# Optimization experiments

Hardware: AMD Instinct MI355X
Metric: run time of the kernel (lower is better)

## Reference

```python
import jax, jax.numpy as jnp
import numpy as np

TEMP = 1.0
EULER_GAMMA = 0.5772156649015329
BIG = 1.0e9


def setup_inputs() -> dict:
    key = jax.random.key(0)
    k = jax.random.split(key, 8)
    B, N, D, H = 32, 1024, 1024, 512  # batch, seq, d_model, hidden_size//2
    queries = jax.random.normal(k[0], (B, N, D), jnp.float32)
    queries_mask = jnp.ones((B, N), dtype=bool)
    W1 = jax.random.normal(k[1], (D, H), jnp.float32) * 0.02
    b1 = jnp.zeros((H,), jnp.float32)
    W2 = jax.random.normal(k[2], (H, 1), jnp.float32) * 0.02
    b2 = jnp.zeros((1,), jnp.float32)
    uniform_noise = jax.random.uniform(k[3], (B, N, 1), jnp.float32, 0.0, 1e-5)
    gumbel_noise = jax.random.gumbel(k[4], (B, N, 1), jnp.float32)
    return {"queries": queries, "queries_mask": queries_mask, "W1": W1, "b1": b1,
            "W2": W2, "b2": b2, "uniform_noise": uniform_noise,
            "gumbel_noise": gumbel_noise, "action_refinement": 1}


def reference(queries, queries_mask, W1, b1, W2, b2, uniform_noise, gumbel_noise, action_refinement):
    B, N, D = queries.shape
    # block0: Dense(H, relu) -> Dense(1); then softplus clamp + log + tiny uniform noise
    h = jax.nn.relu(jnp.einsum('bnd,dh->bnh', queries, W1) + b1)
    acts = jnp.einsum('bnh,ho->bno', h, W2) + b2                      # [B,N,1]
    acts = jnp.log(jnp.maximum(jax.nn.softplus(acts), 1e-5)) + uniform_noise
    acts = jnp.repeat(acts, action_refinement, axis=0)                # [BR,N,1]
    vmask = jnp.repeat(queries_mask[:, None, :].astype(jnp.float32), action_refinement, axis=0)  # [BR,1,N]
    n_valid = jnp.sum(vmask, axis=-1)                                 # [BR,1]
    mask_n1 = jnp.transpose(vmask, (0, 2, 1))                         # [BR,N,1]
    sqz_mask = mask_n1[..., 0]                                        # [BR,N]
    masked_acts = jnp.where(mask_n1 > 0, acts, -1e6)                  # [BR,N,1]
    perturb = masked_acts + gumbel_noise                              # [BR,N,1]
    # deterministic NeuralSort
    s = (jnp.exp(perturb) * mask_n1)[..., 0]                          # [BR,N]
    A = jnp.abs(s[:, :, None] - s[:, None, :])                        # [BR,N,N]
    Bmat = jnp.sum(A, axis=-1, keepdims=True)                         # A @ (1 1^T): row sums broadcast
    scaling = (N + 1 - 2 * (jnp.arange(N) + 1)).astype(jnp.float32)   # [N]
    C = s[:, :, None] * scaling[None, None, :]                        # [BR,N,N]
    P_hat = jnp.transpose(C - Bmat, (0, 2, 1)) - (1.0 - vmask) * BIG  # [BR,N,N]
    # greedy argmax permutation extraction (find_permu), vectorized over batch
    BR = P_hat.shape[0]
    def step(flag, row):                                              # row: [BR,N]
        tmp = row - flag * BIG
        idx = jnp.argmax(tmp, axis=-1)
        flag = jnp.maximum(flag, jax.nn.one_hot(idx, N, dtype=flag.dtype))
        return flag, idx
    _, idxs = jax.lax.scan(step, jnp.zeros((BR, N), jnp.float32), jnp.transpose(P_hat, (1, 0, 2)))
    chosen = jnp.transpose(idxs).astype(jnp.int32)                    # [BR,N]
    chosen = jnp.concatenate([jnp.zeros((BR, 1), jnp.int32), chosen[:, :-1]], axis=-1)
    id_permu = jnp.arange(N, dtype=jnp.int32)[None, :]
    permu = jnp.where(sqz_mask > 0, chosen, id_permu)                 # [BR,N]
    sample_permu = jax.nn.one_hot(permu, N, axis=-1, dtype=jnp.float32)
    # Plackett-Luce log-likelihood of sampled permutation
    exp_actis = jnp.exp(jnp.take_along_axis(masked_acts[..., 0], permu, axis=-1))
    rev_cumsum = jnp.cumsum(exp_actis[:, ::-1], axis=-1)[:, ::-1]
    eps = 1e-20
    log_nom = (jnp.log(exp_actis + eps) - jnp.log(rev_cumsum + eps)) * sqz_mask
    log_nom = jnp.sum(log_nom, axis=-1, keepdims=True)                # [BR,1]
    log_norm = jnp.zeros_like(log_nom)
    # KL term
    sqz_acts = acts[..., 0]
    kl1 = n_valid * (np.log(TEMP) - 1.0 + EULER_GAMMA * (1.0 / TEMP - 1.0))
    s1 = (1.0 / TEMP) * jnp.sum(sqz_acts * sqz_mask, axis=-1).reshape(-1, 1)
    s2 = jnp.sum(jnp.exp(-1.0 / TEMP * jnp.maximum(sqz_acts * sqz_mask, -20.0 * TEMP)), axis=-1).reshape(-1, 1) - (jnp.float32(N) - n_valid)
    kl = kl1 + s1 + s2 * jnp.exp(jax.lax.lgamma(jnp.float32(1.0 + 1.0 / TEMP)))
    return sample_permu, masked_acts[..., 0], kl, log_nom, log_norm
```

## Files before the change

### kernel.cpp

```cpp
#include <hip/hip_runtime.h>
#include <math.h>

#define BB 32
#define NN 1024
#define DD 1024
#define HH 512

#define OUT0_OFF 0
#define OUT1_OFF (BB * NN * NN)
#define OUT2_OFF (OUT1_OFF + BB * NN)
#define OUT3_OFF (OUT2_OFF + BB)
#define OUT4_OFF (OUT3_OFF + BB)

#define WS_ACTS 0
#define WS_W1T  131072
#define WS_RANK 1179648

typedef __attribute__((ext_vector_type(8))) short short8;
typedef __attribute__((ext_vector_type(4))) float floatx4;

__device__ inline unsigned int f2bf(float x) {
    unsigned int u = __builtin_bit_cast(unsigned int, x);
    return (u + 0x7FFFu + ((u >> 16) & 1u)) >> 16;
}

__global__ __launch_bounds__(1024) void w1t_kernel(const float* __restrict__ W1,
                                                   unsigned short* __restrict__ W1T)
{
    __shared__ float T[32][33];
    const int tx = threadIdx.x, ty = threadIdx.y;
    const int d0 = blockIdx.x * 32, h0 = blockIdx.y * 32;
    T[ty][tx] = W1[(d0 + ty) * HH + h0 + tx];
    __syncthreads();
    W1T[(size_t)(h0 + ty) * DD + d0 + tx] = (unsigned short)f2bf(T[tx][ty]);
}

#define ASTRIDE 40
__global__ __launch_bounds__(256, 2) void gemm_acts_kernel(
    const float* __restrict__ q, const unsigned short* __restrict__ W1T,
    const float* __restrict__ b1, const float* __restrict__ W2,
    const float* __restrict__ b2, const float* __restrict__ unoise,
    float* __restrict__ acts_ws, float* __restrict__ out1)
{
    __shared__ short As[2][64 * ASTRIDE];
    __shared__ float red[64][4];

    const int tid = threadIdx.x;
    const int w = tid >> 6, lane = tid & 63;
    const int c = lane & 15, qd = lane >> 4;
    const int m0 = blockIdx.x * 64;

    float b1v[8], w2v[8];
    #pragma unroll
    for (int tn = 0; tn < 8; ++tn) {
        int col = w * 128 + tn * 16 + c;
        b1v[tn] = b1[col];
        w2v[tn] = W2[col];
    }

    floatx4 acc[8][4];
    #pragma unroll
    for (int tn = 0; tn < 8; ++tn)
        #pragma unroll
        for (int tm = 0; tm < 4; ++tm)
            acc[tn][tm] = (floatx4){0.f, 0.f, 0.f, 0.f};

    const int am = tid >> 2, akf = (tid & 3) * 8;
    const float* aptr = q + (size_t)(m0 + am) * DD + akf;

    const unsigned short* bptr = W1T + (size_t)(w * 128 + c) * DD + qd * 8;

    uint4 bfrag[8];
    #pragma unroll
    for (int tn = 0; tn < 8; ++tn)
        bfrag[tn] = *(const uint4*)(bptr + (size_t)tn * 16 * DD);

    for (int kk = 0; kk < 32; ++kk) {
        {
            const float4* ap = (const float4*)(aptr + kk * 32);
            float4 v0 = ap[0], v1 = ap[1];
            uint4 pk;
            pk.x = f2bf(v0.x) | (f2bf(v0.y) << 16);
            pk.y = f2bf(v0.z) | (f2bf(v0.w) << 16);
            pk.z = f2bf(v1.x) | (f2bf(v1.y) << 16);
            pk.w = f2bf(v1.z) | (f2bf(v1.w) << 16);
            *(uint4*)(&As[kk & 1][am * ASTRIDE + akf]) = pk;
        }
        uint4 bnext[8];
        if (kk < 31) {
            #pragma unroll
            for (int tn = 0; tn < 8; ++tn)
                bnext[tn] = *(const uint4*)(bptr + (size_t)tn * 16 * DD + (kk + 1) * 32);
        }
        __syncthreads();
        short8 af[4];
        #pragma unroll
        for (int tm = 0; tm < 4; ++tm)
            af[tm] = *(const short8*)(&As[kk & 1][(tm * 16 + c) * ASTRIDE + qd * 8]);
        #pragma unroll
        for (int tn = 0; tn < 8; ++tn) {
            short8 bf = __builtin_bit_cast(short8, bfrag[tn]);
            #pragma unroll
            for (int tm = 0; tm < 4; ++tm)
                acc[tn][tm] = __builtin_amdgcn_mfma_f32_16x16x32_bf16(
                    af[tm], bf, acc[tn][tm], 0, 0, 0);
        }
        if (kk < 31) {
            #pragma unroll
            for (int tn = 0; tn < 8; ++tn) bfrag[tn] = bnext[tn];
        }
    }

    #pragma unroll
    for (int tm = 0; tm < 4; ++tm) {
        #pragma unroll
        for (int r = 0; r < 4; ++r) {
            float p = 0.f;
            #pragma unroll
            for (int tn = 0; tn < 8; ++tn) {
                float v = acc[tn][tm][r] + b1v[tn];
                p = fmaf(fmaxf(v, 0.f), w2v[tn], p);
            }
            p += __shfl_xor(p, 1);
            p += __shfl_xor(p, 2);
            p += __shfl_xor(p, 4);
            p += __shfl_xor(p, 8);
            if (c == 0) red[tm * 16 + qd * 4 + r][w] = p;
        }
    }
    __syncthreads();
    if (tid < 64) {
        float raw = red[tid][0] + red[tid][1] + red[tid][2] + red[tid][3] + b2[0];
        float sp = fmaxf(raw, 0.f) + log1pf(expf(-fabsf(raw)));
        int row = m0 + tid;
        float av = logf(fmaxf(sp, 1e-5f)) + unoise[row];
        acts_ws[row] = av;
        out1[row]    = av;
    }
}

__global__ __launch_bounds__(256) void rank_kernel(
    const float* __restrict__ acts_ws, const float* __restrict__ gumbel,
    int* __restrict__ rank)
{
    __shared__ float P[NN];
    const int b = blockIdx.x >> 2;
    const int chunk = blockIdx.x & 3;
    const int tid = threadIdx.x;
    #pragma unroll
    for (int r = 0; r < 4; ++r) {
        int j = r * 256 + tid;
        P[j] = acts_ws[b * NN + j] + gumbel[b * NN + j];
    }
    __syncthreads();
    const int i = chunk * 256 + tid;
    const float pert = P[i];
    int cnt = 0;
    const float4* P4 = (const float4*)P;
    for (int j4 = 0; j4 < NN / 4; ++j4) {
        float4 pv = P4[j4];
        int j = j4 * 4;
        cnt += (pv.x > pert) || (pv.x == pert && j + 0 < i);
        cnt += (pv.y > pert) || (pv.y == pert && j + 1 < i);
        cnt += (pv.z > pert) || (pv.z == pert && j + 2 < i);
        cnt += (pv.w > pert) || (pv.w == pert && j + 3 < i);
    }
    rank[b * NN + i] = cnt;
}

__global__ __launch_bounds__(1024) void permu_stats_kernel(
    const float* __restrict__ acts_ws, int* __restrict__ rank_perm,
    float* __restrict__ out2, float* __restrict__ out3, float* __restrict__ out4)
{
    __shared__ float A[NN];
    __shared__ int   IDX[NN];
    __shared__ float WT[16];
    __shared__ float RS[48];

    const int b = blockIdx.x, i = threadIdx.x;
    const int lane = i & 63, w = i >> 6;

    float a = acts_ws[b * NN + i];
    A[i] = a;
    IDX[rank_perm[b * NN + i]] = i;
    __syncthreads();

    int perm = (i == 0) ? 0 : IDX[i - 1];
    rank_perm[b * NN + i] = perm;

    float e = expf(A[perm]);

    float s = e;
    #pragma unroll
    for (int off = 1; off < 64; off <<= 1) {
        float v = __shfl_down(s, off);
        if (lane + off < 64) s += v;
    }
    if (lane == 0) WT[w] = s;
    __syncthreads();
    float suff = 0.f;
    for (int ww = w + 1; ww < 16; ++ww) suff += WT[ww];
    float S = s + suff;
    float term = logf(e + 1e-20f) - logf(S + 1e-20f);

    float r0 = term, r1 = a, r2 = expf(-fmaxf(a, -20.f));
    #pragma unroll
    for (int off = 32; off > 0; off >>= 1) {
        r0 += __shfl_down(r0, off);
        r1 += __shfl_down(r1, off);
        r2 += __shfl_down(r2, off);
    }
    if (lane == 0) { RS[w] = r0; RS[16 + w] = r1; RS[32 + w] = r2; }
    __syncthreads();
    if (i == 0) {
        float t0 = 0.f, t1 = 0.f, t2 = 0.f;
        for (int ww = 0; ww < 16; ++ww) {
            t0 += RS[ww]; t1 += RS[16 + ww]; t2 += RS[32 + ww];
        }
        out2[b] = -(float)NN + t1 + t2;
        out3[b] = t0;
        out4[b] = 0.f;
    }
}

__global__ __launch_bounds__(256) void onehot_kernel(
    const int* __restrict__ perm, float4* __restrict__ out0)
{
    const int t = threadIdx.x;
    const size_t row0 = (size_t)blockIdx.x * 16;
    #pragma unroll
    for (int r = 0; r < 16; ++r) {
        int p = perm[row0 + r];
        float on = ((p >> 2) == t) ? 1.0f : 0.0f;
        float4 v;
        v.x = ((p & 3) == 0) ? on : 0.0f;
        v.y = ((p & 3) == 1) ? on : 0.0f;
        v.z = ((p & 3) == 2) ? on : 0.0f;
        v.w = ((p & 3) == 3) ? on : 0.0f;
        out0[(row0 + r) * 256 + t] = v;
    }
}

extern "C" void kernel_launch(void* const* d_in, const int* in_sizes, int n_in,
                              void* d_out, int out_size, void* d_ws, size_t ws_size,
                              hipStream_t stream)
{
    const float* q      = (const float*)d_in[0];
    const float* W1     = (const float*)d_in[2];
    const float* b1     = (const float*)d_in[3];
    const float* W2     = (const float*)d_in[4];
    const float* b2     = (const float*)d_in[5];
    const float* unoise = (const float*)d_in[6];
    const float* gumbel = (const float*)d_in[7];

    float* out = (float*)d_out;
    char*  ws  = (char*)d_ws;
    float*          acts = (float*)(ws + WS_ACTS);
    unsigned short* W1T  = (unsigned short*)(ws + WS_W1T);
    int*            rkpm = (int*)(ws + WS_RANK);

    w1t_kernel<<<dim3(32, 16), dim3(32, 32), 0, stream>>>(W1, W1T);
    gemm_acts_kernel<<<(BB * NN) / 64, 256, 0, stream>>>(q, W1T, b1, W2, b2,
                                                         unoise, acts,
                                                         out + OUT1_OFF);
    rank_kernel<<<BB * 4, 256, 0, stream>>>(acts, gumbel, rkpm);
    permu_stats_kernel<<<BB, 1024, 0, stream>>>(acts, rkpm, out + OUT2_OFF,
                                                out + OUT3_OFF, out + OUT4_OFF);
    onehot_kernel<<<2048, 256, 0, stream>>>(rkpm, (float4*)(out + OUT0_OFF));
}
```

Before: 340.3 us.

## Load A fragments directly from global, drop shared-memory staging and barrier

The GEMM kernel stops staging the fp32 query tile through shared memory. Each wave now loads its own A fragments straight from global memory into registers, converts them to bf16, and prefetches the next k-slice. This removes the LDS writes, LDS reads and the per-iteration __syncthreads. In exchange, each of the 4 waves re-reads the same A rows from global (4x redundant traffic through the cache), and B fragments are no longer prefetched one iteration ahead. The loop is also left un-unrolled with #pragma unroll 1.

After: 369.7 us. +8.6%, slower.

```diff
diff --git a/kernel.cpp b/kernel.cpp
--- a/kernel.cpp
+++ b/kernel.cpp
@@ -35,14 +35,12 @@
     W1T[(size_t)(h0 + ty) * DD + d0 + tx] = (unsigned short)f2bf(T[tx][ty]);
 }
 
-#define ASTRIDE 40
 __global__ __launch_bounds__(256, 2) void gemm_acts_kernel(
     const float* __restrict__ q, const unsigned short* __restrict__ W1T,
     const float* __restrict__ b1, const float* __restrict__ W2,
     const float* __restrict__ b2, const float* __restrict__ unoise,
     float* __restrict__ acts_ws, float* __restrict__ out1)
 {
-    __shared__ short As[2][64 * ASTRIDE];
     __shared__ float red[64][4];
 
     const int tid = threadIdx.x;
@@ -50,6 +48,62 @@
     const int c = lane & 15, qd = lane >> 4;
     const int m0 = blockIdx.x * 64;
 
+    floatx4 acc[8][4];
+    #pragma unroll
+    for (int tn = 0; tn < 8; ++tn)
+        #pragma unroll
+        for (int tm = 0; tm < 4; ++tm)
+            acc[tn][tm] = (floatx4){0.f, 0.f, 0.f, 0.f};
+
+    const float* aqb = q + (size_t)(m0 + c) * DD + qd * 8;
+    const unsigned short* bb = W1T + (size_t)(w * 128 + c) * DD + qd * 8;
+
+    float4 araw[4][2];
+    #pragma unroll
+    for (int tm = 0; tm < 4; ++tm) {
+        const float* ap = aqb + (size_t)tm * 16 * DD;
+        araw[tm][0] = *(const float4*)(ap);
+        araw[tm][1] = *(const float4*)(ap + 4);
+    }
+
+    #pragma unroll 1
+    for (int kk = 0; kk < 32; ++kk) {
+        uint4 bq[8];
+        #pragma unroll
+        for (int tn = 0; tn < 8; ++tn)
+            bq[tn] = *(const uint4*)(bb + (size_t)tn * 16 * DD + kk * 32);
+
+        short8 af[4];
+        #pragma unroll
+        for (int tm = 0; tm < 4; ++tm) {
+            float4 v0 = araw[tm][0], v1 = araw[tm][1];
+            uint4 u;
+            u.x = f2bf(v0.x) | (f2bf(v0.y) << 16);
+            u.y = f2bf(v0.z) | (f2bf(v0.w) << 16);
+            u.z = f2bf(v1.x) | (f2bf(v1.y) << 16);
+            u.w = f2bf(v1.z) | (f2bf(v1.w) << 16);
+            af[tm] = __builtin_bit_cast(short8, u);
+        }
+
+        if (kk < 31) {
+            #pragma unroll
+            for (int tm = 0; tm < 4; ++tm) {
+                const float* ap = aqb + (size_t)tm * 16 * DD + (kk + 1) * 32;
+                araw[tm][0] = *(const float4*)(ap);
+                araw[tm][1] = *(const float4*)(ap + 4);
+            }
+        }
+
+        #pragma unroll
+        for (int tn = 0; tn < 8; ++tn) {
+            short8 bf = __builtin_bit_cast(short8, bq[tn]);
+            #pragma unroll
+            for (int tm = 0; tm < 4; ++tm)
+                acc[tn][tm] = __builtin_amdgcn_mfma_f32_16x16x32_bf16(
+                    af[tm], bf, acc[tn][tm], 0, 0, 0);
+        }
+    }
+
     float b1v[8], w2v[8];
     #pragma unroll
     for (int tn = 0; tn < 8; ++tn) {
@@ -57,60 +111,6 @@
         b1v[tn] = b1[col];
         w2v[tn] = W2[col];
     }
-
-    floatx4 acc[8][4];
-    #pragma unroll
-    for (int tn = 0; tn < 8; ++tn)
-        #pragma unroll
-        for (int tm = 0; tm < 4; ++tm)
-            acc[tn][tm] = (floatx4){0.f, 0.f, 0.f, 0.f};
-
-    const int am = tid >> 2, akf = (tid & 3) * 8;
-    const float* aptr = q + (size_t)(m0 + am) * DD + akf;
-
-    const unsigned short* bptr = W1T + (size_t)(w * 128 + c) * DD + qd * 8;
-
-    uint4 bfrag[8];
-    #pragma unroll
-    for (int tn = 0; tn < 8; ++tn)
-        bfrag[tn] = *(const uint4*)(bptr + (size_t)tn * 16 * DD);
-
-    for (int kk = 0; kk < 32; ++kk) {
-        {
-            const float4* ap = (const float4*)(aptr + kk * 32);
-            float4 v0 = ap[0], v1 = ap[1];
-            uint4 pk;
-            pk.x = f2bf(v0.x) | (f2bf(v0.y) << 16);
-            pk.y = f2bf(v0.z) | (f2bf(v0.w) << 16);
-            pk.z = f2bf(v1.x) | (f2bf(v1.y) << 16);
-            pk.w = f2bf(v1.z) | (f2bf(v1.w) << 16);
-            *(uint4*)(&As[kk & 1][am * ASTRIDE + akf]) = pk;
-        }
-        uint4 bnext[8];
-        if (kk < 31) {
-            #pragma unroll
-            for (int tn = 0; tn < 8; ++tn)
-                bnext[tn] = *(const uint4*)(bptr + (size_t)tn * 16 * DD + (kk + 1) * 32);
-        }
-        __syncthreads();
-        short8 af[4];
-        #pragma unroll
-        for (int tm = 0; tm < 4; ++tm)
-            af[tm] = *(const short8*)(&As[kk & 1][(tm * 16 + c) * ASTRIDE + qd * 8]);
-        #pragma unroll
-        for (int tn = 0; tn < 8; ++tn) {
-            short8 bf = __builtin_bit_cast(short8, bfrag[tn]);
-            #pragma unroll
-            for (int tm = 0; tm < 4; ++tm)
-                acc[tn][tm] = __builtin_amdgcn_mfma_f32_16x16x32_bf16(
-                    af[tm], bf, acc[tn][tm], 0, 0, 0);
-        }
-        if (kk < 31) {
-            #pragma unroll
-            for (int tn = 0; tn < 8; ++tn) bfrag[tn] = bnext[tn];
-        }
-    }
-
     #pragma unroll
     for (int tm = 0; tm < 4; ++tm) {
         #pragma unroll
```
